# Kernel optimization log

Hardware: AMD Instinct MI355X
Metric: run time of the kernel (lower is better)

## Reference

```python
import jax, jax.numpy as jnp
import numpy as np

NCLASSES = 80
MAX_BOXES = 100
IOU_THR = 0.5
SCORE_THR = 0.0
NEG = -1e9


def arrange_bbox(xy, wh):
    # xy, wh: [1, H, W, 3, 2]
    H, W = xy.shape[1], xy.shape[2]
    gx, gy = jnp.meshgrid(jnp.arange(W), jnp.arange(H))  # 'xy' indexing, each [H, W]
    grid = jnp.stack([gx, gy], axis=-1)[:, :, None, :].astype(xy.dtype)  # [H, W, 1, 2]
    gsize = jnp.array([H, W], dtype=xy.dtype)  # TF divides last dim [x, y] by [H, W]
    xy = (xy + grid) / gsize
    return jnp.concatenate([xy - wh / 2, xy + wh / 2], axis=-1)  # [1,H,W,3,4]


def hard_nms(boxes, scores):
    # boxes: [N,4] (x1,y1,x2,y2); scores: [N]. Greedy NMS, fixed MAX_BOXES output.
    areas = (boxes[:, 2] - boxes[:, 0]) * (boxes[:, 3] - boxes[:, 1])  # [N]

    def step(sw, _):
        j = jnp.argmax(sw)
        s = sw[j]
        valid = s > SCORE_THR
        bj = boxes[j]
        iw = jnp.clip(jnp.minimum(boxes[:, 2], bj[2]) - jnp.maximum(boxes[:, 0], bj[0]), 0.0)
        ih = jnp.clip(jnp.minimum(boxes[:, 3], bj[3]) - jnp.maximum(boxes[:, 1], bj[1]), 0.0)
        inter = iw * ih
        iou = inter / (areas + areas[j] - inter)
        sw = jnp.where((iou > IOU_THR) & valid, NEG, sw)  # suppresses j itself too
        return sw, (jnp.where(valid, j, -1), jnp.where(valid, s, 0.0), valid)

    _, (sel_idx, sel_scores, valids) = jax.lax.scan(step, scores, None, length=MAX_BOXES)
    return sel_idx, sel_scores, valids


def decode(grid0, grid1, grid2, anchors_table):
    outs = (grid0, grid1, grid2)
    anch = (anchors_table[2], anchors_table[1], anchors_table[0])
    bbs, confs, probs = [], [], []
    for g, a in zip(outs, anch):
        xy, wh, obj, cp = jnp.split(g, [2, 4, 5], axis=-1)
        b = arrange_bbox(xy, jnp.exp(wh) * a)
        bbs.append(b.reshape(1, -1, 4))
        confs.append(obj.reshape(1, -1, 1))
        probs.append(cp.reshape(1, -1, NCLASSES))
    bbox = jnp.concatenate(bbs, axis=1).reshape(-1, 4)          # [N,4]
    conf = jnp.concatenate(confs, axis=1)[0, :, 0]              # [N]
    cp = jnp.concatenate(probs, axis=1)[0]                      # [N,C]
    cls_idx = jnp.argmax(cp, axis=-1)                           # [N]
    maxprob = jnp.max(cp, axis=-1)                              # [N]
    # TF code broadcasts conf[1,N,1]*maxprob[N] -> [N,N], then reduce_max over axis 1.
    # Mathematically: scores[i] = max_j conf[i]*maxprob[j] = max(conf*max(mp), conf*min(mp)).
    scores = jnp.maximum(conf * jnp.max(maxprob), conf * jnp.min(maxprob))
    return bbox, scores, cls_idx


def reference(grid0, grid1, grid2, anchors_table):
    bbox, scores, cls_idx = decode(grid0, grid1, grid2, anchors_table)
    sel_idx, sel_scores, valids = hard_nms(bbox, scores)
    safe = jnp.clip(sel_idx, 0)
    sel_boxes = jnp.where(valids[:, None], bbox[safe], 0.0)[None]      # [1,MAX,4]
    sel_scores = sel_scores[None]                                       # [1,MAX]
    sel_classes = jnp.where(valids, cls_idx[safe], 0)[None]            # [1,MAX]
    num_valid = jnp.sum(valids).astype(jnp.int32)[None]                # [1]
    return sel_boxes, sel_scores, sel_classes, num_valid


def setup_inputs() -> dict:
    key = jax.random.key(0)
    k0, k1, k2 = jax.random.split(key, 3)
    grid0 = jax.random.normal(k0, (1, 48, 48, 3, 85), jnp.float32)
    grid1 = jax.random.normal(k1, (1, 96, 96, 3, 85), jnp.float32)
    grid2 = jax.random.normal(k2, (1, 192, 192, 3, 85), jnp.float32)
    anchors = np.array([[[10, 13], [16, 30], [33, 23]],
                        [[30, 61], [62, 45], [59, 119]],
                        [[116, 90], [156, 198], [373, 326]]], np.float32) / 416.0
    return {"grid0": grid0, "grid1": grid1, "grid2": grid2,
            "anchors_table": jnp.asarray(anchors)}
```

## Files before the change

### kernel.cpp

```cpp
#include <hip/hip_runtime.h>
#include <hip/hip_bf16.h>
#include <math.h>


#define NCLS  80
#define MAXB  100
#define N0    6912
#define N1    27648
#define NTOT  145152
#define NTILE 2268
#define NB    4096
#define CAP   2048
#define CAPL  2048
#define CHUNK 256
#define NEGF  -3.402823466e38f
#define POSF   3.402823466e38f

#define WS_CONF 0
#define WS_SCAL (NTOT * 4)
#define WS_PART (WS_SCAL + 16)
#define WS_HIST (WS_PART + NTILE * 16)
#define WS_BINC (WS_HIST + 8 * NB * 4)
#define WS_SUF  (WS_BINC + NB * 4)
#define WS_META (WS_SUF + (NB + 2) * 4)
#define WS_CAND (WS_META + 16)

__device__ __forceinline__ int binOf(float s, float Smax) {
    int b = (int)((s / Smax) * (float)NB);
    return b > (NB - 1) ? (NB - 1) : b;
}
__device__ __forceinline__ float smaxOf(const float* scal) {
    float Mx = scal[0], Mn = scal[1], cmx = scal[2], cmn = scal[3];
    return fmaxf(fmaxf(cmx * Mx, cmx * Mn), fmaxf(cmn * Mx, cmn * Mn));
}
__device__ __forceinline__ float rdlane(float v, int l) {
    return __uint_as_float(__builtin_amdgcn_readlane(__float_as_uint(v), l));
}
__device__ __forceinline__ void decodeBox(int idx, const float* __restrict__ g0,
        const float* __restrict__ g1, const float* __restrict__ g2,
        const float* __restrict__ anch,
        float& x1, float& y1, float& x2, float& y2) {
    const float* g; int H, ar, j;
    if (idx < N0)           { g = g0; H = 48;  ar = 2; j = idx; }
    else if (idx < N0 + N1) { g = g1; H = 96;  ar = 1; j = idx - N0; }
    else                    { g = g2; H = 192; ar = 0; j = idx - N0 - N1; }
    const float* r = g + (size_t)j * 85;
    float tx = r[0], ty = r[1], tw = r[2], th = r[3];
    int cell = j / 3, a = j - cell * 3;
    int hh = cell / H, ww = cell - hh * H;
    float xc = (tx + (float)ww) / (float)H;
    float yc = (ty + (float)hh) / (float)H;
    float bw = expf(tw) * anch[ar * 6 + a * 2];
    float bh = expf(th) * anch[ar * 6 + a * 2 + 1];
    x1 = xc - bw * 0.5f; y1 = yc - bh * 0.5f;
    x2 = xc + bw * 0.5f; y2 = yc + bh * 0.5f;
}

__global__ __launch_bounds__(256) void k_decode(
        const float* __restrict__ g0, const float* __restrict__ g1,
        const float* __restrict__ g2, float* __restrict__ conf,
        float* __restrict__ part) {
    __shared__ float sm[5440];
    __shared__ float red[16];
    const int tid = threadIdx.x;
    const int tile = blockIdx.x;
    const float* p; int ibase, lt;
    if (tile < 108)      { p = g0; ibase = 0;       lt = tile; }
    else if (tile < 540) { p = g1; ibase = N0;      lt = tile - 108; }
    else                 { p = g2; ibase = N0 + N1; lt = tile - 540; }
    const float4* src = (const float4*)(p + (size_t)lt * 5440);
    for (int w = tid; w < 1360; w += 256) ((float4*)sm)[w] = src[w];
    __syncthreads();

    const int b = tid >> 2, pp = tid & 3;
    const float* row = sm + b * 85;
    float best = row[5 + pp * 20];
    #pragma unroll
    for (int k = 1; k < 20; k++) best = fmaxf(best, row[5 + pp * 20 + k]);
    best = fmaxf(best, __shfl_xor(best, 1));
    best = fmaxf(best, __shfl_xor(best, 2));
    float cmx = NEGF, cmn = POSF;
    if (pp == 0) {
        float obj = row[4];
        conf[ibase + lt * 64 + b] = obj;
        cmx = obj; cmn = obj;
    }
    float mpmax = best, mpmin = best;
    for (int off = 32; off; off >>= 1) {
        mpmax = fmaxf(mpmax, __shfl_down(mpmax, off));
        mpmin = fminf(mpmin, __shfl_down(mpmin, off));
        cmx   = fmaxf(cmx,   __shfl_down(cmx,   off));
        cmn   = fminf(cmn,   __shfl_down(cmn,   off));
    }
    const int lane = tid & 63, wid = tid >> 6;
    if (lane == 0) {
        red[wid * 4 + 0] = mpmax; red[wid * 4 + 1] = mpmin;
        red[wid * 4 + 2] = cmx;   red[wid * 4 + 3] = cmn;
    }
    __syncthreads();
    if (tid == 0) {
        float a0 = red[0], a1 = red[1], a2 = red[2], a3 = red[3];
        for (int w = 1; w < 4; w++) {
            a0 = fmaxf(a0, red[w * 4 + 0]); a1 = fminf(a1, red[w * 4 + 1]);
            a2 = fmaxf(a2, red[w * 4 + 2]); a3 = fminf(a3, red[w * 4 + 3]);
        }
        part[tile * 4 + 0] = a0; part[tile * 4 + 1] = a1;
        part[tile * 4 + 2] = a2; part[tile * 4 + 3] = a3;
    }
}

__global__ __launch_bounds__(256) void k_reduce(const float* __restrict__ part,
                                                float* __restrict__ scal) {
    __shared__ float red[16];
    const int tid = threadIdx.x;
    float a0 = NEGF, a1 = POSF, a2 = NEGF, a3 = POSF;
    for (int b = tid; b < NTILE; b += 256) {
        float4 p4 = ((const float4*)part)[b];
        a0 = fmaxf(a0, p4.x); a1 = fminf(a1, p4.y);
        a2 = fmaxf(a2, p4.z); a3 = fminf(a3, p4.w);
    }
    for (int off = 32; off; off >>= 1) {
        a0 = fmaxf(a0, __shfl_down(a0, off)); a1 = fminf(a1, __shfl_down(a1, off));
        a2 = fmaxf(a2, __shfl_down(a2, off)); a3 = fminf(a3, __shfl_down(a3, off));
    }
    const int lane = tid & 63, wid = tid >> 6;
    if (lane == 0) {
        red[wid * 4 + 0] = a0; red[wid * 4 + 1] = a1;
        red[wid * 4 + 2] = a2; red[wid * 4 + 3] = a3;
    }
    __syncthreads();
    if (tid == 0) {
        for (int w = 1; w < 4; w++) {
            a0 = fmaxf(a0, red[w * 4 + 0]); a1 = fminf(a1, red[w * 4 + 1]);
            a2 = fmaxf(a2, red[w * 4 + 2]); a3 = fminf(a3, red[w * 4 + 3]);
        }
        scal[0] = a0; scal[1] = a1; scal[2] = a2; scal[3] = a3;
    }
}

__global__ __launch_bounds__(256) void k_hist(const float* __restrict__ conf,
                                              const float* __restrict__ scal,
                                              int* __restrict__ hist) {
    int i = blockIdx.x * 256 + threadIdx.x;
    float Mx = scal[0], Mn = scal[1];
    float Smax = smaxOf(scal);
    float c = conf[i];
    float s = fmaxf(c * Mx, c * Mn);
    if (s > 0.0f && Smax > 0.0f)
        atomicAdd(&hist[((blockIdx.x & 7) << 12) + binOf(s, Smax)], 1);
}

__global__ __launch_bounds__(1024) void k_thresh(const int* __restrict__ hist,
                                                 int* __restrict__ suf,
                                                 int* __restrict__ meta) {
    __shared__ int grp[1024];
    const int tid = threadIdx.x;
    int b0 = tid * 4;
    int h[4];
    #pragma unroll
    for (int q = 0; q < 4; q++) {
        int s = 0;
        #pragma unroll
        for (int sh = 0; sh < 8; sh++) s += hist[sh * NB + b0 + q];
        h[q] = s;
    }
    grp[tid] = h[0] + h[1] + h[2] + h[3];
    __syncthreads();
    for (int d = 1; d < 1024; d <<= 1) {
        int add = (tid + d < 1024) ? grp[tid + d] : 0;
        __syncthreads();
        grp[tid] += add;
        __syncthreads();
    }
    int gnext = (tid + 1 < 1024) ? grp[tid + 1] : 0;
    suf[b0 + 3] = gnext + h[3];
    suf[b0 + 2] = gnext + h[3] + h[2];
    suf[b0 + 1] = gnext + h[3] + h[2] + h[1];
    suf[b0 + 0] = gnext + h[3] + h[2] + h[1] + h[0];
    if (tid == 0) suf[NB] = 0;
    __syncthreads();
    if (tid == 0) {
        int L = 0, R = NB - 1, res = NB - 1;
        while (L <= R) {
            int m = (L + R) >> 1;
            if (suf[m] <= CAP) { res = m; R = m - 1; } else L = m + 1;
        }
        meta[0] = res;
    }
}

__global__ __launch_bounds__(256) void k_compact(
        const float* __restrict__ conf, const float* __restrict__ scal,
        const int* __restrict__ suf, const int* __restrict__ meta,
        int* __restrict__ binCtr, unsigned long long* __restrict__ cand) {
    int i = blockIdx.x * 256 + threadIdx.x;
    float Mx = scal[0], Mn = scal[1];
    float Smax = smaxOf(scal);
    float c = conf[i];
    float s = fmaxf(c * Mx, c * Mn);
    int lo = meta[0];
    if (s > 0.0f && Smax > 0.0f) {
        int b = binOf(s, Smax);
        if (b >= lo) {
            int pos = suf[b + 1] + atomicAdd(&binCtr[b], 1);
            if (pos < CAP)
                cand[pos] = ((unsigned long long)__float_as_uint(s) << 32)
                          | (unsigned long long)(~(unsigned)i);
        }
    }
}

__global__ __launch_bounds__(64) void k_nms(
        const float* __restrict__ g0, const float* __restrict__ g1,
        const float* __restrict__ g2, const float* __restrict__ anch,
        const float* __restrict__ conf, const float* __restrict__ scal,
        const int* __restrict__ suf, const int* __restrict__ meta,
        const unsigned long long* __restrict__ cand, float* __restrict__ out) {
    __shared__ unsigned long long keys[CAPL];
    __shared__ float selX1[MAXB], selY1[MAXB], selX2[MAXB], selY2[MAXB],
                     selA[MAXB], selS[MAXB];
    __shared__ int selIdx[MAXB];
    __shared__ int sh_cnt;

    const int lane = threadIdx.x;
    const float Mx = scal[0], Mn = scal[1];
    const float Smax = smaxOf(scal);
    const int loGlob = meta[0];
    int nsel = 0;
    int hi = NB;

    while (nsel < MAXB && hi > 0) {
        const bool fast = hi > loGlob;
        const int sufHi = suf[hi];
        int l;
        {
            int lb = fast ? loGlob : 0;
            int capHere = fast ? CHUNK : CAPL;
            int L = lb, R = hi - 1, res = hi - 1;
            while (L <= R) {
                int m = (L + R) >> 1;
                if (suf[m] - sufHi <= capHere) { res = m; R = m - 1; } else L = m + 1;
            }
            l = res;
        }
        int cnt;
        if (fast) {
            cnt = suf[l] - sufHi;
            for (int i = lane; i < cnt; i += 64) keys[i] = cand[sufHi + i];
        } else {
            if (lane == 0) sh_cnt = 0;
            __syncthreads();
            for (int i = lane; i < NTOT; i += 64) {
                float c = conf[i];
                float s = fmaxf(c * Mx, c * Mn);
                if (s > 0.0f) {
                    int b = binOf(s, Smax);
                    if (b >= l && b < hi) {
                        int pos = atomicAdd(&sh_cnt, 1);
                        if (pos < CAPL)
                            keys[pos] = ((unsigned long long)__float_as_uint(s) << 32)
                                      | (unsigned long long)(~(unsigned)i);
                    }
                }
            }
            __syncthreads();
            cnt = sh_cnt; if (cnt > CAPL) cnt = CAPL;
        }
        if (cnt > 0) {
            int n = 2; while (n < cnt) n <<= 1;
            for (int i = cnt + lane; i < n; i += 64) keys[i] = 0ULL;
            __syncthreads();
            for (int k = 2; k <= n; k <<= 1) {
                for (int j = k >> 1; j > 0; j >>= 1) {
                    int half = n >> 1;
                    for (int t = lane; t < half; t += 64) {
                        int i = ((t & ~(j - 1)) << 1) | (t & (j - 1));
                        int ixj = i | j;
                        unsigned long long ka = keys[i], kb = keys[ixj];
                        if ((ka < kb) == ((i & k) == 0)) { keys[i] = kb; keys[ixj] = ka; }
                    }
                    __syncthreads();
                }
            }
            for (int bpos = 0; bpos < cnt && nsel < MAXB; bpos += 64) {
                int t = bpos + lane;
                bool alive = (t < cnt);
                float x1 = 0.f, y1 = 0.f, x2 = 0.f, y2 = 0.f, area = 0.f, sc = 0.f;
                int idx = 0;
                if (alive) {
                    unsigned long long key = keys[t];
                    idx = (int)(~(unsigned)key);
                    sc = __uint_as_float((unsigned)(key >> 32));
                    decodeBox(idx, g0, g1, g2, anch, x1, y1, x2, y2);
                    area = (x2 - x1) * (y2 - y1);
                    for (int s2 = 0; s2 < nsel; s2++) {
                        float iw = fminf(x2, selX2[s2]) - fmaxf(x1, selX1[s2]);
                        float ih = fminf(y2, selY2[s2]) - fmaxf(y1, selY1[s2]);
                        iw = fmaxf(iw, 0.f); ih = fmaxf(ih, 0.f);
                        float inter = iw * ih;
                        if (inter / (area + selA[s2] - inter) > 0.5f) { alive = false; break; }
                    }
                }
                while (nsel < MAXB) {
                    unsigned long long bal = __ballot(alive);
                    if (!bal) break;
                    int w = __ffsll((unsigned long long)bal) - 1;
                    float wx1 = rdlane(x1, w), wy1 = rdlane(y1, w);
                    float wx2 = rdlane(x2, w), wy2 = rdlane(y2, w);
                    float wa  = rdlane(area, w);
                    if (lane == w) {
                        selX1[nsel] = x1; selY1[nsel] = y1;
                        selX2[nsel] = x2; selY2[nsel] = y2;
                        selA[nsel] = area; selS[nsel] = sc; selIdx[nsel] = idx;
                    }
                    if (alive) {
                        float iw = fminf(x2, wx2) - fmaxf(x1, wx1);
                        float ih = fminf(y2, wy2) - fmaxf(y1, wy1);
                        iw = fmaxf(iw, 0.f); ih = fmaxf(ih, 0.f);
                        float inter = iw * ih;
                        if (inter / (area + wa - inter) > 0.5f) alive = false;
                    }
                    nsel++;
                }
                __syncthreads();
            }
        }
        hi = l;
    }
    __syncthreads();

    for (int k = lane; k < MAXB; k += 64) {
        float b0 = 0.f, b1 = 0.f, b2 = 0.f, b3 = 0.f, sv = 0.f, cv = 0.f;
        if (k < nsel) {
            b0 = selX1[k]; b1 = selY1[k]; b2 = selX2[k]; b3 = selY2[k];
            sv = selS[k];
            int idx = selIdx[k];
            const float* g; int j;
            if (idx < N0)           { g = g0; j = idx; }
            else if (idx < N0 + N1) { g = g1; j = idx - N0; }
            else                    { g = g2; j = idx - N0 - N1; }
            const float* r = g + (size_t)j * 85 + 5;
            float v[NCLS];
            #pragma unroll
            for (int q = 0; q < NCLS; q++) v[q] = r[q];
            float best = v[0]; int c = 0;
            #pragma unroll
            for (int q = 1; q < NCLS; q++)
                if (v[q] > best) { best = v[q]; c = q; }
            cv = (float)c;
        }
        out[4 * k + 0] = b0; out[4 * k + 1] = b1;
        out[4 * k + 2] = b2; out[4 * k + 3] = b3;
        out[400 + k] = sv;
        out[500 + k] = cv;
    }
    if (lane == 0) out[600] = (float)nsel;
}

extern "C" void kernel_launch(void* const* d_in, const int* in_sizes, int n_in,
                              void* d_out, int out_size, void* d_ws, size_t ws_size,
                              hipStream_t stream) {
    const float* g0   = (const float*)d_in[0];
    const float* g1   = (const float*)d_in[1];
    const float* g2   = (const float*)d_in[2];
    const float* anch = (const float*)d_in[3];
    char* ws = (char*)d_ws;
    float* conf  = (float*)(ws + WS_CONF);
    float* scal  = (float*)(ws + WS_SCAL);
    float* part  = (float*)(ws + WS_PART);
    int*   hist  = (int*)(ws + WS_HIST);
    int*   binc  = (int*)(ws + WS_BINC);
    int*   suf   = (int*)(ws + WS_SUF);
    int*   meta  = (int*)(ws + WS_META);
    unsigned long long* cand = (unsigned long long*)(ws + WS_CAND);
    float* out   = (float*)d_out;

    hipMemsetAsync(ws + WS_HIST, 0, 9 * NB * 4, stream);
    k_decode <<<NTILE, 256, 0, stream>>>(g0, g1, g2, conf, part);
    k_reduce <<<1, 256, 0, stream>>>(part, scal);
    k_hist   <<<NTOT / 256, 256, 0, stream>>>(conf, scal, hist);
    k_thresh <<<1, 1024, 0, stream>>>(hist, suf, meta);
    k_compact<<<NTOT / 256, 256, 0, stream>>>(conf, scal, suf, meta, binc, cand);
    k_nms    <<<1, 64, 0, stream>>>(g0, g1, g2, anch, conf, scal, suf, meta, cand, out);
}
```

Measured before the change: 159.6 us.

## Widen NMS block to 256 threads with rank sort and wave-level greedy selection

The single-block NMS kernel grows from one wavefront to four. The bitonic sort of candidate keys becomes a rank sort in which each thread counts the larger keys and scatters its own key to its rank. Candidates are decoded and pre-filtered against already selected boxes 256 at a time across all waves, and wave 0 then runs the greedy ballot loop with 4 candidates per lane held in registers. This aims to cut the serial latency of the one-block tail, at the cost of quadratic rank-sort work, duplicate-key ties in the rank, and extra block-wide syncs.

```diff
diff --git a/kernel.cpp b/kernel.cpp
--- a/kernel.cpp
+++ b/kernel.cpp
@@ -13,6 +13,7 @@
 #define CAP   2048
 #define CAPL  2048
 #define CHUNK 256
+#define TBLK  256
 #define NEGF  -3.402823466e38f
 #define POSF   3.402823466e38f
 
@@ -35,6 +36,15 @@
 }
 __device__ __forceinline__ float rdlane(float v, int l) {
     return __uint_as_float(__builtin_amdgcn_readlane(__float_as_uint(v), l));
+}
+__device__ __forceinline__ int rdlanei(int v, int l) {
+    return __builtin_amdgcn_readlane(v, l);
+}
+__device__ __forceinline__ float self4(int s, float a0, float a1, float a2, float a3) {
+    return s == 0 ? a0 : (s == 1 ? a1 : (s == 2 ? a2 : a3));
+}
+__device__ __forceinline__ int seli4(int s, int a0, int a1, int a2, int a3) {
+    return s == 0 ? a0 : (s == 1 ? a1 : (s == 2 ? a2 : a3));
 }
 __device__ __forceinline__ void decodeBox(int idx, const float* __restrict__ g0,
         const float* __restrict__ g1, const float* __restrict__ g2,
@@ -210,19 +220,23 @@
     }
 }
 
-__global__ __launch_bounds__(64) void k_nms(
+__global__ __launch_bounds__(TBLK) void k_nms(
         const float* __restrict__ g0, const float* __restrict__ g1,
         const float* __restrict__ g2, const float* __restrict__ anch,
         const float* __restrict__ conf, const float* __restrict__ scal,
         const int* __restrict__ suf, const int* __restrict__ meta,
         const unsigned long long* __restrict__ cand, float* __restrict__ out) {
     __shared__ unsigned long long keys[CAPL];
-    __shared__ float selX1[MAXB], selY1[MAXB], selX2[MAXB], selY2[MAXB],
-                     selA[MAXB], selS[MAXB];
-    __shared__ int selIdx[MAXB];
-    __shared__ int sh_cnt;
-
-    const int lane = threadIdx.x;
+    __shared__ float4 boxI[TBLK];
+    __shared__ float  areaI[TBLK], scoreI[TBLK];
+    __shared__ int    idxI[TBLK], aliveI[TBLK];
+    __shared__ float4 selBox[MAXB];
+    __shared__ float  selA[MAXB], selS[MAXB];
+    __shared__ int    selIdx[MAXB];
+    __shared__ int    sh_cnt, sh_nsel;
+
+    const int tid = threadIdx.x;
+    const int lane = tid & 63, wid = tid >> 6;
     const float Mx = scal[0], Mn = scal[1];
     const float Smax = smaxOf(scal);
     const int loGlob = meta[0];
@@ -246,11 +260,12 @@
         int cnt;
         if (fast) {
             cnt = suf[l] - sufHi;
-            for (int i = lane; i < cnt; i += 64) keys[i] = cand[sufHi + i];
+            for (int i = tid; i < cnt; i += TBLK) keys[i] = cand[sufHi + i];
+            __syncthreads();
         } else {
-            if (lane == 0) sh_cnt = 0;
+            if (tid == 0) sh_cnt = 0;
             __syncthreads();
-            for (int i = lane; i < NTOT; i += 64) {
+            for (int i = tid; i < NTOT; i += TBLK) {
                 float c = conf[i];
                 float s = fmaxf(c * Mx, c * Mn);
                 if (s > 0.0f) {
@@ -267,72 +282,111 @@
             cnt = sh_cnt; if (cnt > CAPL) cnt = CAPL;
         }
         if (cnt > 0) {
-            int n = 2; while (n < cnt) n <<= 1;
-            for (int i = cnt + lane; i < n; i += 64) keys[i] = 0ULL;
-            __syncthreads();
-            for (int k = 2; k <= n; k <<= 1) {
-                for (int j = k >> 1; j > 0; j >>= 1) {
-                    int half = n >> 1;
-                    for (int t = lane; t < half; t += 64) {
-                        int i = ((t & ~(j - 1)) << 1) | (t & (j - 1));
-                        int ixj = i | j;
-                        unsigned long long ka = keys[i], kb = keys[ixj];
-                        if ((ka < kb) == ((i & k) == 0)) { keys[i] = kb; keys[ixj] = ka; }
-                    }
-                    __syncthreads();
-                }
+            if (cnt <= TBLK) {
+                unsigned long long mk = (tid < cnt) ? keys[tid] : 0ULL;
+                int rank = 0;
+                #pragma unroll 8
+                for (int j = 0; j < cnt; j++) rank += (keys[j] > mk) ? 1 : 0;
+                __syncthreads();
+                if (tid < cnt) keys[rank] = mk;
+                __syncthreads();
+            } else {
+                unsigned long long mk[8]; int rk[8];
+                #pragma unroll
+                for (int q = 0; q < 8; q++) {
+                    int ii = tid + (q << 8);
+                    mk[q] = (ii < cnt) ? keys[ii] : 0ULL;
+                    rk[q] = 0;
+                }
+                for (int j = 0; j < cnt; j++) {
+                    unsigned long long kj = keys[j];
+                    #pragma unroll
+                    for (int q = 0; q < 8; q++) rk[q] += (kj > mk[q]) ? 1 : 0;
+                }
+                __syncthreads();
+                #pragma unroll
+                for (int q = 0; q < 8; q++) {
+                    int ii = tid + (q << 8);
+                    if (ii < cnt) keys[rk[q]] = mk[q];
+                }
+                __syncthreads();
             }
-            for (int bpos = 0; bpos < cnt && nsel < MAXB; bpos += 64) {
-                int t = bpos + lane;
-                bool alive = (t < cnt);
-                float x1 = 0.f, y1 = 0.f, x2 = 0.f, y2 = 0.f, area = 0.f, sc = 0.f;
-                int idx = 0;
-                if (alive) {
-                    unsigned long long key = keys[t];
+            for (int t0 = 0; t0 < cnt && nsel < MAXB; t0 += TBLK) {
+                int tcnt = cnt - t0; if (tcnt > TBLK) tcnt = TBLK;
+                float x1 = 0.f, y1 = 0.f, x2 = 0.f, y2 = 0.f, ar = 0.f, sc = 0.f;
+                int idx = 0, alive = 0;
+                if (tid < tcnt) {
+                    unsigned long long key = keys[t0 + tid];
                     idx = (int)(~(unsigned)key);
                     sc = __uint_as_float((unsigned)(key >> 32));
                     decodeBox(idx, g0, g1, g2, anch, x1, y1, x2, y2);
-                    area = (x2 - x1) * (y2 - y1);
+                    ar = (x2 - x1) * (y2 - y1);
+                    alive = 1;
                     for (int s2 = 0; s2 < nsel; s2++) {
-                        float iw = fminf(x2, selX2[s2]) - fmaxf(x1, selX1[s2]);
-                        float ih = fminf(y2, selY2[s2]) - fmaxf(y1, selY1[s2]);
+                        float4 sb = selBox[s2];
+                        float sa = selA[s2];
+                        float iw = fminf(x2, sb.z) - fmaxf(x1, sb.x);
+                        float ih = fminf(y2, sb.w) - fmaxf(y1, sb.y);
                         iw = fmaxf(iw, 0.f); ih = fmaxf(ih, 0.f);
                         float inter = iw * ih;
-                        if (inter / (area + selA[s2] - inter) > 0.5f) { alive = false; break; }
+                        if (inter / (ar + sa - inter) > 0.5f) { alive = 0; break; }
                     }
                 }
-                while (nsel < MAXB) {
-                    unsigned long long bal = __ballot(alive);
-                    if (!bal) break;
-                    int w = __ffsll((unsigned long long)bal) - 1;
-                    float wx1 = rdlane(x1, w), wy1 = rdlane(y1, w);
-                    float wx2 = rdlane(x2, w), wy2 = rdlane(y2, w);
-                    float wa  = rdlane(area, w);
-                    if (lane == w) {
-                        selX1[nsel] = x1; selY1[nsel] = y1;
-                        selX2[nsel] = x2; selY2[nsel] = y2;
-                        selA[nsel] = area; selS[nsel] = sc; selIdx[nsel] = idx;
+                boxI[tid] = make_float4(x1, y1, x2, y2);
+                areaI[tid] = ar; scoreI[tid] = sc; idxI[tid] = idx; aliveI[tid] = alive;
+                __syncthreads();
+                if (wid == 0) {
+                    float cx1[4], cy1[4], cx2[4], cy2[4], car[4], csc[4];
+                    int cid[4], am = 0;
+                    #pragma unroll
+                    for (int q = 0; q < 4; q++) {
+                        int ci = (lane << 2) + q;
+                        float4 b = boxI[ci];
+                        cx1[q] = b.x; cy1[q] = b.y; cx2[q] = b.z; cy2[q] = b.w;
+                        car[q] = areaI[ci]; csc[q] = scoreI[ci]; cid[q] = idxI[ci];
+                        am |= aliveI[ci] << q;
                     }
-                    if (alive) {
-                        float iw = fminf(x2, wx2) - fmaxf(x1, wx1);
-                        float ih = fminf(y2, wy2) - fmaxf(y1, wy1);
-                        iw = fmaxf(iw, 0.f); ih = fmaxf(ih, 0.f);
-                        float inter = iw * ih;
-                        if (inter / (area + wa - inter) > 0.5f) alive = false;
+                    while (nsel < MAXB) {
+                        unsigned long long bal = __ballot(am != 0);
+                        if (!bal) break;
+                        int w = __ffsll(bal) - 1;
+                        int slot = __ffs(rdlanei(am, w)) - 1;
+                        float wx1 = rdlane(self4(slot, cx1[0], cx1[1], cx1[2], cx1[3]), w);
+                        float wy1 = rdlane(self4(slot, cy1[0], cy1[1], cy1[2], cy1[3]), w);
+                        float wx2 = rdlane(self4(slot, cx2[0], cx2[1], cx2[2], cx2[3]), w);
+                        float wy2 = rdlane(self4(slot, cy2[0], cy2[1], cy2[2], cy2[3]), w);
+                        float wa  = rdlane(self4(slot, car[0], car[1], car[2], car[3]), w);
+                        float ws  = rdlane(self4(slot, csc[0], csc[1], csc[2], csc[3]), w);
+                        int   wi  = rdlanei(seli4(slot, cid[0], cid[1], cid[2], cid[3]), w);
+                        if (lane == 0) {
+                            selBox[nsel] = make_float4(wx1, wy1, wx2, wy2);
+                            selA[nsel] = wa; selS[nsel] = ws; selIdx[nsel] = wi;
+                        }
+                        #pragma unroll
+                        for (int q = 0; q < 4; q++) {
+                            float iw = fminf(cx2[q], wx2) - fmaxf(cx1[q], wx1);
+                            float ih = fminf(cy2[q], wy2) - fmaxf(cy1[q], wy1);
+                            iw = fmaxf(iw, 0.f); ih = fmaxf(ih, 0.f);
+                            float inter = iw * ih;
+                            if (inter / (car[q] + wa - inter) > 0.5f) am &= ~(1 << q);
+                        }
+                        nsel++;
                     }
-                    nsel++;
-                }
-                __syncthreads();
+                    if (lane == 0) sh_nsel = nsel;
+                }
+                __syncthreads();
+                nsel = sh_nsel;
             }
         }
         hi = l;
     }
     __syncthreads();
 
-    for (int k = lane; k < MAXB; k += 64) {
+    for (int k = tid; k < MAXB; k += TBLK) {
         float b0 = 0.f, b1 = 0.f, b2 = 0.f, b3 = 0.f, sv = 0.f, cv = 0.f;
         if (k < nsel) {
-            b0 = selX1[k]; b1 = selY1[k]; b2 = selX2[k]; b3 = selY2[k];
+            float4 sb = selBox[k];
+            b0 = sb.x; b1 = sb.y; b2 = sb.z; b3 = sb.w;
             sv = selS[k];
             int idx = selIdx[k];
             const float* g; int j;
@@ -354,7 +408,7 @@
         out[400 + k] = sv;
         out[500 + k] = cv;
     }
-    if (lane == 0) out[600] = (float)nsel;
+    if (tid == 0) out[600] = (float)nsel;
 }
 
 extern "C" void kernel_launch(void* const* d_in, const int* in_sizes, int n_in,
@@ -381,5 +435,5 @@
     k_hist   <<<NTOT / 256, 256, 0, stream>>>(conf, scal, hist);
     k_thresh <<<1, 1024, 0, stream>>>(hist, suf, meta);
     k_compact<<<NTOT / 256, 256, 0, stream>>>(conf, scal, suf, meta, binc, cand);
-    k_nms    <<<1, 64, 0, stream>>>(g0, g1, g2, anch, conf, scal, suf, meta, cand, out);
-}
+    k_nms    <<<1, TBLK, 0, stream>>>(g0, g1, g2, anch, conf, scal, suf, meta, cand, out);
+}
```

Result: slower. 194.3 us (+21.7%).
